# Optimization experiments

Hardware: AMD Instinct MI355X
Metric: run time of the kernel (lower is better)

The kernel has to match this reference:

```python
import jax, jax.numpy as jnp
import numpy as np

B, N, P = 256, 32, 32
OBS, ACT = 96, 32
OBS_P, ACT_P = 96, 32
DIN = OBS + ACT          # obs_act_input_dim = 128
DOUT = 128               # obs_act_output_dim
DIN_P = OBS_P + ACT_P    # obs_act_input_dim_people = 128
DOUT_P = 128             # obs_act_output_dim_people
DF1, DF2 = 64, 32        # final hidden / final_output_dim


def setup_inputs() -> dict:
    key = jax.random.key(0)
    ks = jax.random.split(key, 13)
    s = 0.05
    return {
        "states": jax.random.normal(ks[0], (B, N, OBS), jnp.float32),
        "policies": jax.random.uniform(ks[1], (B, N, ACT), jnp.float32),
        "actions": jax.random.uniform(ks[2], (B, N, ACT), jnp.float32),
        "states_people": jax.random.normal(ks[3], (B, P, OBS_P), jnp.float32),
        "actions_people": jax.random.uniform(ks[4], (B, P, ACT_P), jnp.float32),
        "W_k": jax.random.normal(ks[5], (DIN, DOUT), jnp.float32) * s,
        "W_q": jax.random.normal(ks[6], (DIN, DOUT), jnp.float32) * s,
        "W_v": jax.random.normal(ks[7], (DIN, DOUT), jnp.float32) * s,
        "W_kp": jax.random.normal(ks[8], (DIN_P, DOUT_P), jnp.float32) * s,
        "W_qp": jax.random.normal(ks[9], (DIN, DOUT), jnp.float32) * s,
        "W_vp": jax.random.normal(ks[10], (DIN_P, DOUT_P), jnp.float32) * s,
        "W_f1": jax.random.normal(ks[11], (DOUT + DOUT_P, DF1), jnp.float32) * s,
        "W_f2": jax.random.normal(ks[12], (DF1, DF2), jnp.float32) * s,
    }


def reference(states, policies, actions, states_people, actions_people,
              W_k, W_q, W_v, W_kp, W_qp, W_vp, W_f1, W_f2):
    n = states.shape[1]
    p = states_people.shape[1]
    dk = jnp.asarray(W_k.shape[1], states.dtype)
    dkp = jnp.asarray(W_kp.shape[1], states.dtype)

    oa = jnp.concatenate([states, actions], axis=-1)    # [B,N,DIN]
    op = jnp.concatenate([states, policies], axis=-1)   # [B,N,DIN]

    k = oa @ W_k   # [B,N,DOUT]
    q = oa @ W_q   # [B,N,DOUT]
    scores = jnp.einsum('bid,bjd->bij', q, k)            # [B,N,N]
    # torch path: transpose then softmax over last axis of transposed scores
    weight = jax.nn.softmax(jnp.swapaxes(scores, 1, 2) / jnp.sqrt(dk), axis=-1)  # [B,N,N]

    # place_policies/place_actions masks == identity selector over (i==j)
    eye = jnp.eye(n, dtype=oa.dtype)[None, :, :, None]   # [1,N,N,1]
    oap = eye * op[:, None, :, :] + (1.0 - eye) * oa[:, None, :, :]  # [B,N,N,DIN]
    av = jnp.tanh(oap @ W_v)                             # [B,N,N,DOUT]
    # torch: mean_j( av[b,i,j] * weight[b,a,j] ) -> [B,N(a),N(i),DOUT]
    wav = jnp.einsum('baj,bijd->baid', weight, av) / n

    oa_p = jnp.concatenate([states_people, actions_people], axis=-1)  # [B,P,DIN_P]
    kp = oa_p @ W_kp                                     # [B,P,DOUT_P]
    qp = oa @ W_qp                                       # [B,N,DOUT_P]
    avp = jnp.tanh(oa_p @ W_vp)                          # [B,P,DOUT_P]
    scores_p = jnp.einsum('bnd,bpd->bnp', qp, kp)        # [B,N,P]
    # original softmax over dim=-2 (agents)
    wp = jax.nn.softmax(scores_p / jnp.sqrt(dkp), axis=-2)           # [B,N,P]
    wavp = jnp.einsum('bnp,bpd->bnd', wp, avp) / p       # mean over people

    wavp_b = jnp.broadcast_to(wavp[:, :, None, :], wav.shape[:3] + (wavp.shape[-1],))
    node_features = jnp.concatenate([wav, wavp_b], axis=-1)          # [B,N,N,256]

    h = jax.nn.leaky_relu(node_features @ W_f1)          # slope 0.01 (torch default)
    value = h @ W_f2                                     # [B,N,N,DF2]
    return value, weight, wp[..., None]
```

## Files before the change

kernel.cpp:

```cpp
#include <hip/hip_runtime.h>

#define VAL_SZ  (256*32*32*32)
#define W_OFF   VAL_SZ
#define WP_OFF  (VAL_SZ + 256*32*32)

typedef short  bf16x8 __attribute__((ext_vector_type(8)));
typedef float  f32x4  __attribute__((ext_vector_type(4)));

#define MFMA(a, b, c) __builtin_amdgcn_mfma_f32_16x16x32_bf16(a, b, c, 0, 0, 0)

static __device__ __forceinline__ unsigned short f2bf(float f) {
    union { float f; unsigned u; } v; v.f = f;
    unsigned r = (v.u + 0x7FFF + ((v.u >> 16) & 1)) >> 16;
    return (unsigned short)r;
}
static __device__ __forceinline__ float bf2f(unsigned short u) {
    union { unsigned u; float f; } v; v.u = ((unsigned)u) << 16;
    return v.f;
}
static __device__ __forceinline__ float fast_tanh(float x) {
    x = fminf(fmaxf(x, -12.0f), 12.0f);
    float e = __expf(2.0f * x);
    return (e - 1.0f) / (e + 1.0f);
}

static __device__ __forceinline__ bf16x8 afrag(const unsigned short* Mb, int stride,
                                               int row0, int kt) {
    int lane = threadIdx.x & 63;
    return *(const bf16x8*)(Mb + (row0 + (lane & 15)) * stride + kt * 32 + (lane >> 4) * 8);
}

static __device__ __forceinline__ bf16x8 bfrag_gather(const float* __restrict__ W,
                                                      int ldn, int kt, int nt) {
    int lane = threadIdx.x & 63;
    int l16 = lane & 15, quad = lane >> 4;
    const float* p = W + (kt * 32 + quad * 8) * ldn + nt * 16 + l16;
    union { unsigned short u[8]; bf16x8 v; } o;
#pragma unroll
    for (int j = 0; j < 8; ++j) o.u[j] = f2bf(p[j * ldn]);
    return o.v;
}

__global__ __launch_bounds__(1024) void critic_fused(
    const float* __restrict__ states, const float* __restrict__ policies,
    const float* __restrict__ actions, const float* __restrict__ states_p,
    const float* __restrict__ actions_p,
    const float* __restrict__ Wk, const float* __restrict__ Wq,
    const float* __restrict__ Wv, const float* __restrict__ Wkp,
    const float* __restrict__ Wqp, const float* __restrict__ Wvp,
    const float* __restrict__ Wf1, const float* __restrict__ Wf2,
    float* __restrict__ out)
{
    __shared__ __align__(16) unsigned char SM[64000];
    unsigned short* OA  = (unsigned short*)(SM + 0);
    unsigned short* TD  = (unsigned short*)(SM + 8704);
    unsigned short* NF  = (unsigned short*)(SM + 0);
    unsigned short* OP  = (unsigned short*)(SM + 17408);
    unsigned short* QL  = (unsigned short*)(SM + 26112);
    unsigned short* WPB = (unsigned short*)(SM + 26112);
    float*          FP  = (float*)(SM + 26112);
    unsigned short* KL  = (unsigned short*)(SM + 34816);
    float*          GP  = (float*)(SM + 34816);
    unsigned short* VT  = (unsigned short*)(SM + 43520);
    unsigned short* AVT = (unsigned short*)(SM + 51712);
    unsigned short* SB1 = (unsigned short*)(SM + 59904);
    unsigned short* SB2 = (unsigned short*)(SM + 61952);

    const int tid = threadIdx.x;
    const int b = blockIdx.x;
    const int lane = tid & 63, wv = tid >> 6;
    const int l16 = lane & 15, quad = lane >> 4;
    const float invN = 1.0f / 32.0f;
    const float scale = 0.08838834764831845f;
    const f32x4 Z = {0.f, 0.f, 0.f, 0.f};

    {
        const float* st = states   + (size_t)b * 3072;
        const float* ac = actions  + (size_t)b * 1024;
        const float* po = policies + (size_t)b * 1024;
#pragma unroll
        for (int k = 0; k < 4; ++k) {
            int idx = tid + k * 1024;
            int n = idx >> 7, d = idx & 127;
            float sv, pv;
            if (d < 96) { sv = st[n * 96 + d]; pv = sv; }
            else        { sv = ac[n * 32 + d - 96]; pv = po[n * 32 + d - 96]; }
            OA[n * 136 + d] = f2bf(sv);
            OP[n * 136 + d] = f2bf(pv);
        }
    }
    __syncthreads();

    if (wv < 8) {
        int mt = wv & 1, ntA = wv >> 1, ntB = ntA + 4;
        f32x4 va0 = Z, va1 = Z, vp0 = Z, vp1 = Z;
#pragma unroll
        for (int kt = 0; kt < 4; ++kt) {
            bf16x8 aA = afrag(OA, 136, mt * 16, kt);
            bf16x8 aP = afrag(OP, 136, mt * 16, kt);
            bf16x8 b0 = bfrag_gather(Wv, 128, kt, ntA);
            bf16x8 b1 = bfrag_gather(Wv, 128, kt, ntB);
            va0 = MFMA(aA, b0, va0); va1 = MFMA(aA, b1, va1);
            vp0 = MFMA(aP, b0, vp0); vp1 = MFMA(aP, b1, vp1);
        }
#pragma unroll
        for (int r = 0; r < 4; ++r) {
            int row = mt * 16 + quad * 4 + r;
            float tva0 = fast_tanh(va0[r]), tvp0 = fast_tanh(vp0[r]);
            float tva1 = fast_tanh(va1[r]), tvp1 = fast_tanh(vp1[r]);
            VT[(ntA * 16 + l16) * 32 + row] = f2bf(tva0);
            VT[(ntB * 16 + l16) * 32 + row] = f2bf(tva1);
            TD[row * 136 + ntA * 16 + l16] = f2bf(tvp0 - tva0);
            TD[row * 136 + ntB * 16 + l16] = f2bf(tvp1 - tva1);
        }
    } else {
        int s = wv - 8;
        int mt = s & 1, pb2 = s >> 1;
        bf16x8 afr[4];
#pragma unroll
        for (int kt = 0; kt < 4; ++kt) afr[kt] = afrag(OA, 136, mt * 16, kt);
#pragma unroll
        for (int m2 = 0; m2 < 2; ++m2) {
            const float* W = m2 ? Wk : Wq;
            unsigned short* dst = m2 ? KL : QL;
#pragma unroll
            for (int h = 0; h < 2; ++h) {
                int nt = pb2 + h * 4;
                f32x4 acc = Z;
#pragma unroll
                for (int kt = 0; kt < 4; ++kt)
                    acc = MFMA(afr[kt], bfrag_gather(W, 128, kt, nt), acc);
#pragma unroll
                for (int r = 0; r < 4; ++r)
                    dst[(mt * 16 + quad * 4 + r) * 136 + nt * 16 + l16] = f2bf(acc[r]);
            }
        }
    }
    __syncthreads();

    f32x4 gReg = Z;
    int gmt = 0, gnt = 0;
    if (wv < 8) {
        gmt = wv & 1; gnt = wv >> 1;
#pragma unroll
        for (int kt = 0; kt < 4; ++kt)
            gReg = MFMA(afrag(TD, 136, gmt * 16, kt), bfrag_gather(Wf1, 64, kt, gnt), gReg);
    } else if (wv < 12) {
        int s = wv - 8;
        int mt = s & 1, nt = s >> 1;
        f32x4 acc = Z;
#pragma unroll
        for (int kt = 0; kt < 4; ++kt)
            acc = MFMA(afrag(QL, 136, mt * 16, kt), afrag(KL, 136, nt * 16, kt), acc);
#pragma unroll
        for (int r = 0; r < 4; ++r)
            SB1[(nt * 16 + l16) * 32 + mt * 16 + quad * 4 + r] = f2bf(acc[r]);
    } else {
        const float* st = states_p  + (size_t)b * 3072;
        const float* ac = actions_p + (size_t)b * 1024;
        int t256 = tid - 768;
#pragma unroll
        for (int k = 0; k < 16; ++k) {
            int idx = t256 + k * 256;
            int n = idx >> 7, d = idx & 127;
            OP[n * 136 + d] = f2bf((d < 96) ? st[n * 96 + d] : ac[n * 32 + d - 96]);
        }
    }
    __syncthreads();

    {
        int mt = wv & 1, nt = wv >> 1;
        bf16x8 ao[4], ap[4];
#pragma unroll
        for (int kt = 0; kt < 4; ++kt) {
            ao[kt] = afrag(OA, 136, mt * 16, kt);
            ap[kt] = afrag(OP, 136, mt * 16, kt);
        }
        f32x4 aq = Z, akp = Z, aav = Z;
#pragma unroll
        for (int kt = 0; kt < 4; ++kt) {
            aq  = MFMA(ao[kt], bfrag_gather(Wqp, 128, kt, nt), aq);
            akp = MFMA(ap[kt], bfrag_gather(Wkp, 128, kt, nt), akp);
            aav = MFMA(ap[kt], bfrag_gather(Wvp, 128, kt, nt), aav);
        }
#pragma unroll
        for (int r = 0; r < 4; ++r) {
            int row = mt * 16 + quad * 4 + r;
            QL[row * 136 + nt * 16 + l16] = f2bf(aq[r]);
            KL[row * 136 + nt * 16 + l16] = f2bf(akp[r]);
            AVT[(nt * 16 + l16) * 32 + row] = f2bf(fast_tanh(aav[r]));
        }
    }
    __syncthreads();

    if (wv < 4) {
        int mt = wv & 1, nt = wv >> 1;
        f32x4 acc = Z;
#pragma unroll
        for (int kt = 0; kt < 4; ++kt)
            acc = MFMA(afrag(QL, 136, mt * 16, kt), afrag(KL, 136, nt * 16, kt), acc);
#pragma unroll
        for (int r = 0; r < 4; ++r)
            SB2[(nt * 16 + l16) * 32 + mt * 16 + quad * 4 + r] = f2bf(acc[r]);
    } else if (wv >= 8) {
        int t512 = tid - 512;
#pragma unroll
        for (int rep = 0; rep < 2; ++rep) {
            int idx = t512 + rep * 512;
            int j = idx & 31, a = idx >> 5;
            float x = bf2f(SB1[a * 32 + j]) * scale;
            float m = x;
#pragma unroll
            for (int msk = 16; msk >= 1; msk >>= 1) m = fmaxf(m, __shfl_xor(m, msk));
            float e = __expf(x - m);
            float s = e;
#pragma unroll
            for (int msk = 16; msk >= 1; msk >>= 1) s += __shfl_xor(s, msk);
            float w = e / s;
            out[W_OFF + (size_t)b * 1024 + a * 32 + j] = w;
            SB1[a * 32 + j] = f2bf(w);
        }
    }
    __syncthreads();

    if (wv < 8) {
#pragma unroll
        for (int rep = 0; rep < 2; ++rep) {
            int idx = tid + rep * 512;
            int n = idx & 31, p = idx >> 5;
            float x = bf2f(SB2[p * 32 + n]) * scale;
            float m = x;
#pragma unroll
            for (int msk = 16; msk >= 1; msk >>= 1) m = fmaxf(m, __shfl_xor(m, msk));
            float e = __expf(x - m);
            float s = e;
#pragma unroll
            for (int msk = 16; msk >= 1; msk >>= 1) s += __shfl_xor(s, msk);
            float w2 = e / s;
            out[WP_OFF + (size_t)b * 1024 + n * 32 + p] = w2;
            WPB[n * 32 + p] = f2bf(w2);
        }
    } else {
        int s = wv - 8;
        int mt = s & 1, nt0 = s >> 1, nt1 = nt0 + 4;
        bf16x8 aw = afrag(SB1, 32, mt * 16, 0);
        f32x4 s0 = MFMA(aw, afrag(VT, 32, nt0 * 16, 0), Z);
        f32x4 s1 = MFMA(aw, afrag(VT, 32, nt1 * 16, 0), Z);
#pragma unroll
        for (int r = 0; r < 4; ++r) {
            int row = mt * 16 + quad * 4 + r;
            NF[row * 264 + nt0 * 16 + l16] = f2bf(s0[r] * invN);
            NF[row * 264 + nt1 * 16 + l16] = f2bf(s1[r] * invN);
        }
    }
    __syncthreads();

    {
        int mt = wv & 1, nt = wv >> 1;
        f32x4 acc = MFMA(afrag(WPB, 32, mt * 16, 0), afrag(AVT, 32, nt * 16, 0), Z);
#pragma unroll
        for (int r = 0; r < 4; ++r) {
            int row = mt * 16 + quad * 4 + r;
            NF[row * 264 + 128 + nt * 16 + l16] = f2bf(acc[r] * invN);
        }
    }
    __syncthreads();

    if (wv < 8) {
        int mt = wv & 1, nt = wv >> 1;
        f32x4 f = Z;
#pragma unroll
        for (int kt = 0; kt < 8; ++kt)
            f = MFMA(afrag(NF, 264, mt * 16, kt), bfrag_gather(Wf1, 64, kt, nt), f);
#pragma unroll
        for (int r = 0; r < 4; ++r) {
            FP[(mt * 16 + quad * 4 + r) * 66 + nt * 16 + l16] = f[r];
            GP[(gmt * 16 + quad * 4 + r) * 67 + gnt * 16 + l16] = gReg[r];
        }
    }
    __syncthreads();

    {
        bf16x8 bw[2][2];
#pragma unroll
        for (int kt = 0; kt < 2; ++kt)
#pragma unroll
            for (int nt = 0; nt < 2; ++nt)
                bw[kt][nt] = bfrag_gather(Wf2, 32, kt, nt);

#pragma unroll
        for (int t4 = 0; t4 < 4; ++t4) {
            int tile = wv + t4 * 16;
            int m0 = tile * 16;
            int a = m0 >> 5;
            int i = (m0 & 31) + l16;
            float w = bf2f(SB1[a * 32 + i]) * invN;
            const float* Fa = FP + a * 66;
            const float* Gi = GP + i * 67;
            f32x4 acc0 = Z, acc1 = Z;
#pragma unroll
            for (int kt = 0; kt < 2; ++kt) {
                union { unsigned short u[8]; bf16x8 v; } h;
                int dbase = kt * 32 + quad * 8;
#pragma unroll
                for (int j = 0; j < 8; ++j) {
                    float z = fmaf(w, Gi[dbase + j], Fa[dbase + j]);
                    z = fmaxf(z, 0.01f * z);
                    h.u[j] = f2bf(z);
                }
                acc0 = MFMA(h.v, bw[kt][0], acc0);
                acc1 = MFMA(h.v, bw[kt][1], acc1);
            }
            float* base = out + (size_t)b * 32768 + (size_t)m0 * 32;
#pragma unroll
            for (int r = 0; r < 4; ++r) {
                int row = quad * 4 + r;
                base[row * 32 + l16]      = acc0[r];
                base[row * 32 + 16 + l16] = acc1[r];
            }
        }
    }
}

extern "C" void kernel_launch(void* const* d_in, const int* in_sizes, int n_in,
                              void* d_out, int out_size, void* d_ws, size_t ws_size,
                              hipStream_t stream)
{
    const float* states    = (const float*)d_in[0];
    const float* policies  = (const float*)d_in[1];
    const float* actions   = (const float*)d_in[2];
    const float* states_p  = (const float*)d_in[3];
    const float* actions_p = (const float*)d_in[4];
    const float* Wk        = (const float*)d_in[5];
    const float* Wq        = (const float*)d_in[6];
    const float* Wv        = (const float*)d_in[7];
    const float* Wkp       = (const float*)d_in[8];
    const float* Wqp       = (const float*)d_in[9];
    const float* Wvp       = (const float*)d_in[10];
    const float* Wf1       = (const float*)d_in[11];
    const float* Wf2       = (const float*)d_in[12];
    float* out = (float*)d_out;

    critic_fused<<<256, 1024, 0, stream>>>(states, policies, actions,
                                           states_p, actions_p,
                                           Wk, Wq, Wv, Wkp, Wqp, Wvp,
                                           Wf1, Wf2, out);
}
```

Before: 115.1 us.

## Prepack weights into bf16 MFMA fragment layout with a separate pre-kernel

Adds a small kernel that converts every weight matrix to bf16 once per call and stores it in the exact per-lane MFMA B-fragment order in the workspace. The main kernel then loads each fragment with one 16-byte vector read instead of eight strided fp32 loads plus conversions. The softmax scale is folded into the packed Wq and Wqp. This removes redundant per-block gathers and conversions, repeated across 256 blocks, at the cost of one extra kernel launch and a workspace round trip.

```diff
diff --git a/kernel.cpp b/kernel.cpp
--- a/kernel.cpp
+++ b/kernel.cpp
@@ -3,6 +3,15 @@
 #define VAL_SZ  (256*32*32*32)
 #define W_OFF   VAL_SZ
 #define WP_OFF  (VAL_SZ + 256*32*32)
+
+#define PK_WV   0
+#define PK_WVP  16384
+#define PK_WQ   32768
+#define PK_WK   49152
+#define PK_WQP  65536
+#define PK_WKP  81920
+#define PK_WF1  98304
+#define PK_WF2  114688
 
 typedef short  bf16x8 __attribute__((ext_vector_type(8)));
 typedef float  f32x4  __attribute__((ext_vector_type(4)));
@@ -30,26 +39,59 @@
     return *(const bf16x8*)(Mb + (row0 + (lane & 15)) * stride + kt * 32 + (lane >> 4) * 8);
 }
 
-static __device__ __forceinline__ bf16x8 bfrag_gather(const float* __restrict__ W,
-                                                      int ldn, int kt, int nt) {
+static __device__ __forceinline__ bf16x8 bfrag_pk(const unsigned short* base, int NT,
+                                                  int kt, int nt) {
     int lane = threadIdx.x & 63;
+    return *(const bf16x8*)(base + (((kt * NT + nt) * 64) + lane) * 8);
+}
+
+__global__ __launch_bounds__(256) void pack_lite(
+    const float* __restrict__ Wk, const float* __restrict__ Wq,
+    const float* __restrict__ Wv, const float* __restrict__ Wkp,
+    const float* __restrict__ Wqp, const float* __restrict__ Wvp,
+    const float* __restrict__ Wf1, const float* __restrict__ Wf2,
+    unsigned short* __restrict__ pk)
+{
+    const float scale = 0.08838834764831845f;
+    int gid = blockIdx.x * 256 + threadIdx.x;
+    if (gid >= 14592) return;
+
+    const float* W; int off, NT, ldn; float s = 1.0f;
+    int r;
+    if (gid < 12288) {
+        int mat = gid >> 11;
+        r = gid & 2047;
+        NT = 8; ldn = 128;
+        switch (mat) {
+            case 0: W = Wv;  off = PK_WV;  break;
+            case 1: W = Wvp; off = PK_WVP; break;
+            case 2: W = Wq;  off = PK_WQ;  s = scale; break;
+            case 3: W = Wk;  off = PK_WK;  break;
+            case 4: W = Wqp; off = PK_WQP; s = scale; break;
+            default: W = Wkp; off = PK_WKP; break;
+        }
+    } else if (gid < 14336) {
+        r = gid - 12288; W = Wf1; off = PK_WF1; NT = 4; ldn = 64;
+    } else {
+        r = gid - 14336; W = Wf2; off = PK_WF2; NT = 2; ldn = 32;
+    }
+    int lane = r & 63;
     int l16 = lane & 15, quad = lane >> 4;
-    const float* p = W + (kt * 32 + quad * 8) * ldn + nt * 16 + l16;
+    int ktnt = r >> 6;
+    int nt = ktnt % NT, kt = ktnt / NT;
+    int n = nt * 16 + l16;
+    int kb = kt * 32 + quad * 8;
     union { unsigned short u[8]; bf16x8 v; } o;
 #pragma unroll
-    for (int j = 0; j < 8; ++j) o.u[j] = f2bf(p[j * ldn]);
-    return o.v;
+    for (int j = 0; j < 8; ++j) o.u[j] = f2bf(W[(kb + j) * ldn + n] * s);
+    *(bf16x8*)(pk + off + (ktnt * 64 + lane) * 8) = o.v;
 }
 
 __global__ __launch_bounds__(1024) void critic_fused(
     const float* __restrict__ states, const float* __restrict__ policies,
     const float* __restrict__ actions, const float* __restrict__ states_p,
     const float* __restrict__ actions_p,
-    const float* __restrict__ Wk, const float* __restrict__ Wq,
-    const float* __restrict__ Wv, const float* __restrict__ Wkp,
-    const float* __restrict__ Wqp, const float* __restrict__ Wvp,
-    const float* __restrict__ Wf1, const float* __restrict__ Wf2,
-    float* __restrict__ out)
+    const unsigned short* __restrict__ pk, float* __restrict__ out)
 {
     __shared__ __align__(16) unsigned char SM[64000];
     unsigned short* OA  = (unsigned short*)(SM + 0);
@@ -71,7 +113,6 @@
     const int lane = tid & 63, wv = tid >> 6;
     const int l16 = lane & 15, quad = lane >> 4;
     const float invN = 1.0f / 32.0f;
-    const float scale = 0.08838834764831845f;
     const f32x4 Z = {0.f, 0.f, 0.f, 0.f};
 
     {
@@ -98,8 +139,8 @@
         for (int kt = 0; kt < 4; ++kt) {
             bf16x8 aA = afrag(OA, 136, mt * 16, kt);
             bf16x8 aP = afrag(OP, 136, mt * 16, kt);
-            bf16x8 b0 = bfrag_gather(Wv, 128, kt, ntA);
-            bf16x8 b1 = bfrag_gather(Wv, 128, kt, ntB);
+            bf16x8 b0 = bfrag_pk(pk + PK_WV, 8, kt, ntA);
+            bf16x8 b1 = bfrag_pk(pk + PK_WV, 8, kt, ntB);
             va0 = MFMA(aA, b0, va0); va1 = MFMA(aA, b1, va1);
             vp0 = MFMA(aP, b0, vp0); vp1 = MFMA(aP, b1, vp1);
         }
@@ -121,7 +162,7 @@
         for (int kt = 0; kt < 4; ++kt) afr[kt] = afrag(OA, 136, mt * 16, kt);
 #pragma unroll
         for (int m2 = 0; m2 < 2; ++m2) {
-            const float* W = m2 ? Wk : Wq;
+            const unsigned short* pkM = pk + (m2 ? PK_WK : PK_WQ);
             unsigned short* dst = m2 ? KL : QL;
 #pragma unroll
             for (int h = 0; h < 2; ++h) {
@@ -129,7 +170,7 @@
                 f32x4 acc = Z;
 #pragma unroll
                 for (int kt = 0; kt < 4; ++kt)
-                    acc = MFMA(afr[kt], bfrag_gather(W, 128, kt, nt), acc);
+                    acc = MFMA(afr[kt], bfrag_pk(pkM, 8, kt, nt), acc);
 #pragma unroll
                 for (int r = 0; r < 4; ++r)
                     dst[(mt * 16 + quad * 4 + r) * 136 + nt * 16 + l16] = f2bf(acc[r]);
@@ -144,7 +185,7 @@
         gmt = wv & 1; gnt = wv >> 1;
 #pragma unroll
         for (int kt = 0; kt < 4; ++kt)
-            gReg = MFMA(afrag(TD, 136, gmt * 16, kt), bfrag_gather(Wf1, 64, kt, gnt), gReg);
+            gReg = MFMA(afrag(TD, 136, gmt * 16, kt), bfrag_pk(pk + PK_WF1, 4, kt, gnt), gReg);
     } else if (wv < 12) {
         int s = wv - 8;
         int mt = s & 1, nt = s >> 1;
@@ -179,9 +220,9 @@
         f32x4 aq = Z, akp = Z, aav = Z;
 #pragma unroll
         for (int kt = 0; kt < 4; ++kt) {
-            aq  = MFMA(ao[kt], bfrag_gather(Wqp, 128, kt, nt), aq);
-            akp = MFMA(ap[kt], bfrag_gather(Wkp, 128, kt, nt), akp);
-            aav = MFMA(ap[kt], bfrag_gather(Wvp, 128, kt, nt), aav);
+            aq  = MFMA(ao[kt], bfrag_pk(pk + PK_WQP, 8, kt, nt), aq);
+            akp = MFMA(ap[kt], bfrag_pk(pk + PK_WKP, 8, kt, nt), akp);
+            aav = MFMA(ap[kt], bfrag_pk(pk + PK_WVP, 8, kt, nt), aav);
         }
 #pragma unroll
         for (int r = 0; r < 4; ++r) {
@@ -208,7 +249,7 @@
         for (int rep = 0; rep < 2; ++rep) {
             int idx = t512 + rep * 512;
             int j = idx & 31, a = idx >> 5;
-            float x = bf2f(SB1[a * 32 + j]) * scale;
+            float x = bf2f(SB1[a * 32 + j]);
             float m = x;
 #pragma unroll
             for (int msk = 16; msk >= 1; msk >>= 1) m = fmaxf(m, __shfl_xor(m, msk));
@@ -228,7 +269,7 @@
         for (int rep = 0; rep < 2; ++rep) {
             int idx = tid + rep * 512;
             int n = idx & 31, p = idx >> 5;
-            float x = bf2f(SB2[p * 32 + n]) * scale;
+            float x = bf2f(SB2[p * 32 + n]);
             float m = x;
 #pragma unroll
             for (int msk = 16; msk >= 1; msk >>= 1) m = fmaxf(m, __shfl_xor(m, msk));
@@ -271,7 +312,7 @@
         f32x4 f = Z;
 #pragma unroll
         for (int kt = 0; kt < 8; ++kt)
-            f = MFMA(afrag(NF, 264, mt * 16, kt), bfrag_gather(Wf1, 64, kt, nt), f);
+            f = MFMA(afrag(NF, 264, mt * 16, kt), bfrag_pk(pk + PK_WF1, 4, kt, nt), f);
 #pragma unroll
         for (int r = 0; r < 4; ++r) {
             FP[(mt * 16 + quad * 4 + r) * 66 + nt * 16 + l16] = f[r];
@@ -286,7 +327,7 @@
         for (int kt = 0; kt < 2; ++kt)
 #pragma unroll
             for (int nt = 0; nt < 2; ++nt)
-                bw[kt][nt] = bfrag_gather(Wf2, 32, kt, nt);
+                bw[kt][nt] = bfrag_pk(pk + PK_WF2, 2, kt, nt);
 
 #pragma unroll
         for (int t4 = 0; t4 < 4; ++t4) {
@@ -340,9 +381,9 @@
     const float* Wf1       = (const float*)d_in[11];
     const float* Wf2       = (const float*)d_in[12];
     float* out = (float*)d_out;
-
+    unsigned short* pk = (unsigned short*)d_ws;
+
+    pack_lite<<<57, 256, 0, stream>>>(Wk, Wq, Wv, Wkp, Wqp, Wvp, Wf1, Wf2, pk);
     critic_fused<<<256, 1024, 0, stream>>>(states, policies, actions,
-                                           states_p, actions_p,
-                                           Wk, Wq, Wv, Wkp, Wqp, Wvp,
-                                           Wf1, Wf2, out);
-}
+                                           states_p, actions_p, pk, out);
+}
```

After: 109.0 us. 5.3% less time.
